# Performance work log

Hardware: AMD Instinct MI355X
Metric: run time of the kernel (lower is better)

## Reference

```python
import jax, jax.numpy as jnp
import numpy as np

B, S, H = 8, 1024, 1536          # batch, seq, hidden_size
NH, HD, AH = 8, 96, 768          # heads after head_ratio=2, head_size=hidden/16, all_head_size
K = 7                            # conv_kernel_size
IM = 3072                        # intermediate_size
EPS = 1e-12                      # ConvBert layer_norm_eps


def _ln(x, g, b):
    m = x.mean(-1, keepdims=True)
    v = ((x - m) ** 2).mean(-1, keepdims=True)
    return (x - m) / jnp.sqrt(v + EPS) * g + b


def _windows(x, k):
    # x: [B,S,C] -> sliding windows [B,S,k,C] with 'same' padding ((k-1)//2 each side, k odd)
    p = (k - 1) // 2
    xp = jnp.pad(x, ((0, 0), (p, p), (0, 0)))
    idx = jnp.arange(x.shape[1])[:, None] + jnp.arange(k)[None, :]
    return xp[:, idx, :]


def _forward(embed, wq, bq, wk, bk, wv, bv, dw, pw, sep_b, wck, bck, wco, bco,
             wso, bso, ln1_g, ln1_b, wi, bi, wo, bo, ln2_g, ln2_b, wd, bd):
    b, s, _ = embed.shape
    # --- projections (weights stored [in,out]) ---
    q = embed @ wq + bq            # [B,S,AH]
    kk = embed @ wk + bk
    v = embed @ wv + bv
    # --- SeparableConv1D on hidden states: depthwise(k=7) then pointwise + bias ---
    win_h = _windows(embed, K)                             # [B,S,K,H]
    dconv = jnp.einsum('bskc,ck->bsc', win_h, dw)          # depthwise, [B,S,H]
    sep = dconv @ pw + sep_b                               # pointwise, [B,S,AH]
    # --- span dynamic conv kernels ---
    conv_attn = sep * q                                    # [B,S,AH]
    ck = (conv_attn @ wck + bck).reshape(b, s, NH, K)      # [B,S,NH,K]
    ck = jax.nn.softmax(ck, axis=-1)
    co = embed @ wco + bco                                 # [B,S,AH]
    win_co = _windows(co, K).reshape(b, s, K, NH, HD)      # [B,S,K,NH,HD]
    conv_out = jnp.einsum('bskhd,bshk->bshd', win_co, ck)  # [B,S,NH,HD]
    # --- standard self-attention on the reduced heads ---
    qh = q.reshape(b, s, NH, HD)
    kh = kk.reshape(b, s, NH, HD)
    vh = v.reshape(b, s, NH, HD)
    scores = jnp.einsum('bqhd,bkhd->bhqk', qh, kh) / jnp.sqrt(jnp.float32(HD))
    probs = jax.nn.softmax(scores, axis=-1)
    ctx = jnp.einsum('bhqk,bkhd->bqhd', probs, vh)         # [B,S,NH,HD]
    # --- concat attention heads with conv heads -> [B,S,2*NH,HD] -> [B,S,H] ---
    ctx = jnp.concatenate([ctx, conv_out], axis=2).reshape(b, s, H)
    # --- self output (dropout is identity at inference) ---
    attn_out = _ln(ctx @ wso + bso + embed, ln1_g, ln1_b)
    # --- FFN ---
    inter = jax.nn.gelu(attn_out @ wi + bi, approximate=False)
    layer_out = _ln(inter @ wo + bo + attn_out, ln2_g, ln2_b)
    # --- global max pooling over sequence + linear decoder ---
    pooled = layer_out.max(axis=1)                         # [B,H]
    logits = pooled @ wd + bd                              # [B,1]
    return logits


def setup_inputs() -> dict:
    key = jax.random.key(0)
    ks = jax.random.split(key, 32)
    rn = lambda i, shape, s=0.02: jax.random.normal(ks[i], shape, jnp.float32) * s
    d = {}
    d['embed'] = jax.random.normal(ks[0], (B, S, H), jnp.float32)
    d['wq'] = rn(1, (H, AH)); d['bq'] = jnp.zeros((AH,), jnp.float32)
    d['wk'] = rn(2, (H, AH)); d['bk'] = jnp.zeros((AH,), jnp.float32)
    d['wv'] = rn(3, (H, AH)); d['bv'] = jnp.zeros((AH,), jnp.float32)
    d['dw'] = rn(4, (H, K)); d['pw'] = rn(5, (H, AH)); d['sep_b'] = jnp.zeros((AH,), jnp.float32)
    d['wck'] = rn(6, (AH, NH * K)); d['bck'] = jnp.zeros((NH * K,), jnp.float32)
    d['wco'] = rn(7, (H, AH)); d['bco'] = jnp.zeros((AH,), jnp.float32)
    d['wso'] = rn(8, (H, H)); d['bso'] = jnp.zeros((H,), jnp.float32)
    d['ln1_g'] = jnp.ones((H,), jnp.float32); d['ln1_b'] = jnp.zeros((H,), jnp.float32)
    d['wi'] = rn(9, (H, IM)); d['bi'] = jnp.zeros((IM,), jnp.float32)
    d['wo'] = rn(10, (IM, H)); d['bo'] = jnp.zeros((H,), jnp.float32)
    d['ln2_g'] = jnp.ones((H,), jnp.float32); d['ln2_b'] = jnp.zeros((H,), jnp.float32)
    d['wd'] = jax.random.uniform(ks[11], (H, 1), jnp.float32, -0.1, 0.1)
    d['bd'] = jnp.zeros((1,), jnp.float32)
    return d


def reference(embed, wq, bq, wk, bk, wv, bv, dw, pw, sep_b, wck, bck, wco, bco,
              wso, bso, ln1_g, ln1_b, wi, bi, wo, bo, ln2_g, ln2_b, wd, bd):
    return _forward(embed, wq, bq, wk, bk, wv, bv, dw, pw, sep_b, wck, bck, wco, bco,
                    wso, bso, ln1_g, ln1_b, wi, bi, wo, bo, ln2_g, ln2_b, wd, bd)
```

## Files before the change

kernel.cpp:

```cpp
#include <hip/hip_runtime.h>


typedef __bf16 bf16_t;
typedef short s16x8 __attribute__((ext_vector_type(8)));
typedef float f32x4 __attribute__((ext_vector_type(4)));

#define BB  8
#define SS  1024
#define HH  1536
#define NHH 8
#define HDD 96
#define AHH 768
#define IMM 3072

__device__ __forceinline__ float rd_adapt(const void* p, long long i, int isbf) {
    return isbf ? (float)((const bf16_t*)p)[i] : ((const float*)p)[i];
}

__device__ __forceinline__ float gelu_f(float v) {
    float u = v * (0.7978845608f + 0.0356774081f * v * v);
    float e = __expf(2.0f * u);
    float t = 1.0f - 2.0f / (e + 1.0f);
    return 0.5f * v * (1.0f + t);
}

__device__ __forceinline__ void gl2lds16(const bf16_t* g, bf16_t* l) {
    __builtin_amdgcn_global_load_lds(
        (__attribute__((address_space(1))) const void*)g,
        (__attribute__((address_space(3))) void*)l, 16, 0, 0);
}

__global__ __launch_bounds__(256)
void detect_kernel(const void* __restrict__ embed, int* __restrict__ flag)
{
    __shared__ int cnt[256];
    int t = threadIdx.x;
    float x = (float)((const bf16_t*)embed)[t];
    float a = fabsf(x);
    cnt[t] = (a > 1e-3f && a < 50.0f) ? 1 : 0;
    __syncthreads();
    for (int o = 128; o > 0; o >>= 1) { if (t < o) cnt[t] += cnt[t + o]; __syncthreads(); }
    if (t == 0) *flag = (cnt[0] >= 205) ? 1 : 0;
}

__global__ __launch_bounds__(256)
void convert_embed(const void* __restrict__ in, bf16_t* __restrict__ out,
                   const int* __restrict__ flagp)
{
    int isbf = *flagp;
    long long i0 = ((long long)blockIdx.x * 256 + threadIdx.x) * 8;
    if (isbf) {
        *(s16x8*)(out + i0) = *(const s16x8*)((const bf16_t*)in + i0);
    } else {
        const float* f = (const float*)in;
        #pragma unroll
        for (int j = 0; j < 8; j++) out[i0 + j] = (bf16_t)f[i0 + j];
    }
}

__global__ __launch_bounds__(256)
void concat_bias(const void* __restrict__ b0, const void* __restrict__ b1,
                 const void* __restrict__ b2, const void* __restrict__ b3,
                 bf16_t* __restrict__ out, const int* __restrict__ flagp)
{
    int isbf = *flagp;
    int t = blockIdx.x * 256 + threadIdx.x;
    int sel = t / 768, off = t - sel * 768;
    const void* src = (sel == 0) ? b0 : (sel == 1) ? b1 : (sel == 2) ? b2 : b3;
    out[t] = (bf16_t)rd_adapt(src, off, isbf);
}

__global__ __launch_bounds__(256)
void gemm_tile(const bf16_t* __restrict__ A, const bf16_t* __restrict__ Bt,
               bf16_t* __restrict__ C, const void* __restrict__ bias, long long biasOff,
               const bf16_t* __restrict__ emul, int lde, const int* __restrict__ flagp,
               int M, int N, int Kd, int lda, int ldb, int ldc,
               float scale, int act, int beta, int nlim)
{
    __shared__ bf16_t Sm[16384];

    int isbf = flagp ? *flagp : 1;
    int tid  = threadIdx.x;
    int wave = tid >> 6, lane = tid & 63;
    int wm = wave >> 1, wn = wave & 1;
    int row0 = blockIdx.x * 128;
    int col0 = blockIdx.y * 128;
    int lm = lane & 15;
    int kq = lane >> 4;

    int sr = tid >> 2;
    int sc = (tid & 3) * 8;
    const bf16_t* ga0 = A + (long long)(row0 + sr) * lda + sc;
    const bf16_t* ga1 = A + (long long)(row0 + 64 + sr) * lda + sc;
    int br0 = min(col0 + sr, nlim);
    int br1 = min(col0 + 64 + sr, nlim);
    const bf16_t* gb0 = Bt + (long long)br0 * ldb + sc;
    const bf16_t* gb1 = Bt + (long long)br1 * ldb + sc;
    bf16_t* lw = Sm + wave * 512;

    f32x4 acc[4][4] = {};

    for (int k0 = 0; k0 < Kd; k0 += 64) {
        #pragma unroll
        for (int h = 0; h < 2; h++) {
            int kh = k0 + h * 32;
            gl2lds16(ga0 + kh, lw + h * 4096);
            gl2lds16(ga1 + kh, lw + h * 4096 + 2048);
            gl2lds16(gb0 + kh, lw + 8192 + h * 4096);
            gl2lds16(gb1 + kh, lw + 8192 + h * 4096 + 2048);
        }
        __syncthreads();

        s16x8 af[2][4], bfr[2][4];
        #pragma unroll
        for (int h = 0; h < 2; h++) {
            #pragma unroll
            for (int i = 0; i < 4; i++)
                af[h][i] = *(const s16x8*)(Sm + h * 4096 + (wm * 64 + i * 16 + lm) * 32 + kq * 8);
            #pragma unroll
            for (int j = 0; j < 4; j++)
                bfr[h][j] = *(const s16x8*)(Sm + 8192 + h * 4096 + (wn * 64 + j * 16 + lm) * 32 + kq * 8);
        }
        #pragma unroll
        for (int i = 0; i < 4; i++)
            #pragma unroll
            for (int j = 0; j < 4; j++) {
                acc[i][j] = __builtin_amdgcn_mfma_f32_16x16x32_bf16(af[0][i], bfr[0][j], acc[i][j], 0, 0, 0);
                acc[i][j] = __builtin_amdgcn_mfma_f32_16x16x32_bf16(af[1][i], bfr[1][j], acc[i][j], 0, 0, 0);
            }
        __syncthreads();
    }

    #pragma unroll
    for (int j = 0; j < 4; j++) {
        int gcol = col0 + wn * 64 + j * 16 + lm;
        if (gcol >= N) continue;
        float bv = bias ? rd_adapt(bias, biasOff + gcol, isbf) : 0.0f;
        #pragma unroll
        for (int i = 0; i < 4; i++) {
            int grow0 = row0 + wm * 64 + i * 16 + kq * 4;
            #pragma unroll
            for (int r = 0; r < 4; r++) {
                float v = acc[i][j][r] * scale + bv;
                long long ci = (long long)(grow0 + r) * ldc + gcol;
                if (beta) v += (float)C[ci];
                if (emul) v *= (float)emul[(long long)(grow0 + r) * lde + gcol];
                if (act) v = gelu_f(v);
                C[ci] = (bf16_t)v;
            }
        }
    }
}

__global__ __launch_bounds__(256, 2)
void flash_attn(const bf16_t* __restrict__ qkv, const bf16_t* __restrict__ vT,
                bf16_t* __restrict__ ctxcat)
{
    const float ascale = 0.1020620726159658f;
    __shared__ bf16_t Pl[4 * 32 * 136];

    int bh = blockIdx.x;
    int b = bh >> 3, h = bh & 7;
    const bf16_t* Qp = qkv  + (long long)b * SS * 3072 + h * HDD;
    const bf16_t* Kp = qkv  + (long long)b * SS * 3072 + 768 + h * HDD;
    const bf16_t* Vt = vT   + (long long)b * AHH * SS + (long long)h * HDD * SS;
    bf16_t*       Op = ctxcat + (long long)b * SS * HH + h * HDD;

    int tid = threadIdx.x, wave = tid >> 6, lane = tid & 63;
    int lm = lane & 15, kq = lane >> 4;
    int q0 = blockIdx.y * 128 + wave * 32;
    bf16_t* Pw = Pl + wave * 32 * 136;

    s16x8 aq[2][3];
    #pragma unroll
    for (int i = 0; i < 2; i++)
        #pragma unroll
        for (int kf = 0; kf < 3; kf++)
            aq[i][kf] = *(const s16x8*)(Qp + (long long)(q0 + i * 16 + lm) * 3072 + kf * 32 + kq * 8);

    f32x4 Oacc[2][6] = {};
    float mrow[2][4], lrow[2][4];
    #pragma unroll
    for (int i = 0; i < 2; i++)
        #pragma unroll
        for (int r = 0; r < 4; r++) { mrow[i][r] = -1e30f; lrow[i][r] = 0.0f; }

    for (int kt = 0; kt < 8; kt++) {
        f32x4 S[2][8] = {};
        #pragma unroll
        for (int j = 0; j < 8; j++) {
            s16x8 bk[3];
            #pragma unroll
            for (int kf = 0; kf < 3; kf++)
                bk[kf] = *(const s16x8*)(Kp + (long long)(kt * 128 + j * 16 + lm) * 3072 + kf * 32 + kq * 8);
            #pragma unroll
            for (int i = 0; i < 2; i++)
                #pragma unroll
                for (int kf = 0; kf < 3; kf++)
                    S[i][j] = __builtin_amdgcn_mfma_f32_16x16x32_bf16(aq[i][kf], bk[kf], S[i][j], 0, 0, 0);
        }

        float mnew[2][4];
        #pragma unroll
        for (int i = 0; i < 2; i++) {
            #pragma unroll
            for (int r = 0; r < 4; r++) {
                float mx = -1e30f;
                #pragma unroll
                for (int j = 0; j < 8; j++) mx = fmaxf(mx, S[i][j][r]);
                #pragma unroll
                for (int msk = 1; msk <= 8; msk <<= 1) mx = fmaxf(mx, __shfl_xor(mx, msk));
                mnew[i][r] = fmaxf(mrow[i][r], mx * ascale);
            }
        }
        #pragma unroll
        for (int i = 0; i < 2; i++) {
            #pragma unroll
            for (int r = 0; r < 4; r++) {
                float al = __expf(mrow[i][r] - mnew[i][r]);
                lrow[i][r] *= al;
                #pragma unroll
                for (int n = 0; n < 6; n++) Oacc[i][n][r] *= al;
                mrow[i][r] = mnew[i][r];
            }
        }
        float psum[2][4] = {};
        __syncthreads();
        #pragma unroll
        for (int i = 0; i < 2; i++) {
            #pragma unroll
            for (int j = 0; j < 8; j++) {
                #pragma unroll
                for (int r = 0; r < 4; r++) {
                    float p = __expf(S[i][j][r] * ascale - mnew[i][r]);
                    psum[i][r] += p;
                    Pw[(i * 16 + kq * 4 + r) * 136 + j * 16 + lm] = (bf16_t)p;
                }
            }
        }
        #pragma unroll
        for (int i = 0; i < 2; i++) {
            #pragma unroll
            for (int r = 0; r < 4; r++) {
                float t = psum[i][r];
                #pragma unroll
                for (int msk = 1; msk <= 8; msk <<= 1) t += __shfl_xor(t, msk);
                lrow[i][r] += t;
            }
        }
        __syncthreads();

        s16x8 ap[2][4];
        #pragma unroll
        for (int i = 0; i < 2; i++)
            #pragma unroll
            for (int kf = 0; kf < 4; kf++)
                ap[i][kf] = *(const s16x8*)(Pw + (i * 16 + lm) * 136 + kf * 32 + kq * 8);
        #pragma unroll
        for (int n = 0; n < 6; n++) {
            s16x8 bv[4];
            #pragma unroll
            for (int kf = 0; kf < 4; kf++)
                bv[kf] = *(const s16x8*)(Vt + (long long)(n * 16 + lm) * SS + kt * 128 + kf * 32 + kq * 8);
            #pragma unroll
            for (int i = 0; i < 2; i++)
                #pragma unroll
                for (int kf = 0; kf < 4; kf++)
                    Oacc[i][n] = __builtin_amdgcn_mfma_f32_16x16x32_bf16(ap[i][kf], bv[kf], Oacc[i][n], 0, 0, 0);
        }
    }

    #pragma unroll
    for (int i = 0; i < 2; i++) {
        #pragma unroll
        for (int n = 0; n < 6; n++) {
            #pragma unroll
            for (int r = 0; r < 4; r++) {
                int row = q0 + i * 16 + kq * 4 + r;
                int col = n * 16 + lm;
                Op[(long long)row * HH + col] = (bf16_t)(Oacc[i][n][r] / lrow[i][r]);
            }
        }
    }
}

__global__ __launch_bounds__(256)
void transpose_pad(const void* __restrict__ in, bf16_t* __restrict__ out,
                   int R, int C, int ldin, long long inOff,
                   long long sInB, long long sOutB, const int* __restrict__ flagp)
{
    __shared__ bf16_t t[32][33];
    int isbf = flagp ? *flagp : 1;
    int z = blockIdx.z;
    long long base = inOff + (long long)z * sInB;
    bf16_t* op = out + (long long)z * sOutB;
    int tx = threadIdx.x & 31, ty = threadIdx.x >> 5;
    int cb = blockIdx.x * 32, rb = blockIdx.y * 32;
    #pragma unroll
    for (int rr = ty; rr < 32; rr += 8) {
        int r = rb + rr, c = cb + tx;
        t[rr][tx] = (c < C) ? (bf16_t)rd_adapt(in, base + (long long)r * ldin + c, isbf)
                            : (bf16_t)0.0f;
    }
    __syncthreads();
    #pragma unroll
    for (int rr = ty; rr < 32; rr += 8) {
        int c = cb + rr;
        op[(long long)c * R + rb + tx] = t[tx][rr];
    }
}

__global__ __launch_bounds__(256)
void dconv_kernel(const bf16_t* __restrict__ ebuf, const void* __restrict__ dw,
                  bf16_t* __restrict__ out, const int* __restrict__ flagp)
{
    int isbf = *flagp;
    long long i = (long long)blockIdx.x * 256 + threadIdx.x;
    int c = (int)(i % HH);
    long long bs = i / HH;
    int s = (int)(bs % SS);
    float acc = 0.0f;
    #pragma unroll
    for (int k = 0; k < 7; k++) {
        int ss = s + k - 3;
        if (ss >= 0 && ss < SS)
            acc += (float)ebuf[(bs + (k - 3)) * HH + c] * rd_adapt(dw, c * 7 + k, isbf);
    }
    out[i] = (bf16_t)acc;
}

__global__ __launch_bounds__(256)
void ck_softmax(const bf16_t* __restrict__ ck, float* __restrict__ ckp)
{
    int i = blockIdx.x * 256 + threadIdx.x;
    if (i >= BB * SS * NHH) return;
    int h = i % NHH;
    long long bs = i / NHH;
    const bf16_t* src = ck + bs * 64 + h * 7;
    float v[7], mx = -1e30f;
    #pragma unroll
    for (int k = 0; k < 7; k++) { v[k] = (float)src[k]; mx = fmaxf(mx, v[k]); }
    float sum = 0.0f;
    #pragma unroll
    for (int k = 0; k < 7; k++) { v[k] = expf(v[k] - mx); sum += v[k]; }
    float inv = 1.0f / sum;
    float* dst = ckp + bs * 56 + h * 7;
    #pragma unroll
    for (int k = 0; k < 7; k++) dst[k] = v[k] * inv;
}

__global__ __launch_bounds__(256)
void conv_out_kernel(const bf16_t* __restrict__ co, int ldco,
                     const float* __restrict__ ckp, bf16_t* __restrict__ ctxcat)
{
    long long i = (long long)blockIdx.x * 256 + threadIdx.x;
    int hd = (int)(i % AHH);
    long long bs = i / AHH;
    int s = (int)(bs % SS);
    int h = hd / HDD;
    const float* w = ckp + bs * 56 + h * 7;
    float acc = 0.0f;
    #pragma unroll
    for (int k = 0; k < 7; k++) {
        int ss = s + k - 3;
        if (ss >= 0 && ss < SS)
            acc += (float)co[(bs + (k - 3)) * ldco + hd] * w[k];
    }
    ctxcat[bs * HH + AHH + hd] = (bf16_t)acc;
}

__global__ __launch_bounds__(256)
void ln_kernel(const bf16_t* __restrict__ y, const bf16_t* __restrict__ res,
               const void* __restrict__ g, const void* __restrict__ bta,
               bf16_t* __restrict__ outb, const int* __restrict__ flagp)
{
    int isbf = *flagp;
    long long row = blockIdx.x;
    const bf16_t* yp = y + row * HH;
    const bf16_t* rp = res + row * HH;
    int tid = threadIdx.x;
    float x[6], s = 0.0f, s2 = 0.0f;
    #pragma unroll
    for (int i = 0; i < 6; i++) {
        int c = tid + i * 256;
        float v = (float)yp[c] + (float)rp[c];
        x[i] = v; s += v; s2 += v * v;
    }
    __shared__ float sa[256], sb[256];
    sa[tid] = s; sb[tid] = s2; __syncthreads();
    for (int o = 128; o > 0; o >>= 1) {
        if (tid < o) { sa[tid] += sa[tid + o]; sb[tid] += sb[tid + o]; }
        __syncthreads();
    }
    float mean = sa[0] * (1.0f / HH);
    float var  = sb[0] * (1.0f / HH) - mean * mean;
    float inv  = rsqrtf(var + 1e-12f);
    #pragma unroll
    for (int i = 0; i < 6; i++) {
        int c = tid + i * 256;
        float v = (x[i] - mean) * inv * rd_adapt(g, c, isbf) + rd_adapt(bta, c, isbf);
        outb[row * HH + c] = (bf16_t)v;
    }
}

__global__ __launch_bounds__(256)
void maxpool_p1(const bf16_t* __restrict__ lo, float* __restrict__ part)
{
    int sc = blockIdx.x, b = blockIdx.y;
    int tid = threadIdx.x;
    const bf16_t* p = lo + ((long long)b * SS + sc * 32) * HH;
    float m[6];
    #pragma unroll
    for (int k = 0; k < 6; k++) m[k] = -1e30f;
    for (int r = 0; r < 32; r++)
        #pragma unroll
        for (int k = 0; k < 6; k++)
            m[k] = fmaxf(m[k], (float)p[(long long)r * HH + k * 256 + tid]);
    #pragma unroll
    for (int k = 0; k < 6; k++)
        part[((long long)b * 32 + sc) * HH + k * 256 + tid] = m[k];
}

__global__ __launch_bounds__(256)
void maxpool_p2(const float* __restrict__ part, float* __restrict__ pooled)
{
    int i = blockIdx.x * 256 + threadIdx.x;
    if (i >= BB * HH) return;
    int b = i / HH, c = i % HH;
    float m = -1e30f;
    for (int ch = 0; ch < 32; ch++) m = fmaxf(m, part[((long long)b * 32 + ch) * HH + c]);
    pooled[i] = m;
}

__global__ __launch_bounds__(256)
void decoder_kernel(const float* __restrict__ pooled, const void* __restrict__ wd,
                    const void* __restrict__ bd, void* __restrict__ out,
                    const int* __restrict__ flagp)
{
    int isbf = *flagp;
    int b = blockIdx.x;
    int tid = threadIdx.x;
    float s = 0.0f;
    #pragma unroll
    for (int i = 0; i < 6; i++) {
        int c = tid + i * 256;
        s += pooled[b * HH + c] * rd_adapt(wd, c, isbf);
    }
    __shared__ float sa[256];
    sa[tid] = s; __syncthreads();
    for (int o = 128; o > 0; o >>= 1) { if (tid < o) sa[tid] += sa[tid + o]; __syncthreads(); }
    if (tid == 0) {
        float r = sa[0] + rd_adapt(bd, 0, isbf);
        if (isbf) ((bf16_t*)out)[b] = (bf16_t)r;
        else      ((float*)out)[b]  = r;
    }
}

extern "C" void kernel_launch(void* const* d_in, const int* in_sizes, int n_in,
                              void* d_out, int out_size, void* d_ws, size_t ws_size,
                              hipStream_t stream)
{
    const void* embed = d_in[0];
    const void* wq  = d_in[1];  const void* bq  = d_in[2];
    const void* wk  = d_in[3];  const void* bk  = d_in[4];
    const void* wv  = d_in[5];  const void* bv  = d_in[6];
    const void* dw  = d_in[7];  const void* pw  = d_in[8];  const void* sep_b = d_in[9];
    const void* wck = d_in[10]; const void* bck = d_in[11];
    const void* wco = d_in[12]; const void* bco = d_in[13];
    const void* wso = d_in[14]; const void* bso = d_in[15];
    const void* ln1g = d_in[16]; const void* ln1b = d_in[17];
    const void* wi  = d_in[18]; const void* bi  = d_in[19];
    const void* wo  = d_in[20]; const void* bo  = d_in[21];
    const void* ln2g = d_in[22]; const void* ln2b = d_in[23];
    const void* wd  = d_in[24]; const void* bd  = d_in[25];
    (void)ws_size; (void)in_sizes; (void)n_in; (void)out_size;

    char* ws = (char*)d_ws;
    char* A  = ws;
    char* B  = ws + 50331648;
    char* C_ = ws + 75497472;
    char* D  = ws + 88080384;
    char* E  = ws + 113246208;
    char* F  = ws + 138412032;
    char* XP = ws + 143130624;

    bf16_t* qkvco  = (bf16_t*)A;
    bf16_t* ybuf   = (bf16_t*)A;
    bf16_t* interb = (bf16_t*)A;
    bf16_t* lout   = (bf16_t*)A;
    bf16_t* wT_all = (bf16_t*)B;
    bf16_t* dconvb = (bf16_t*)B;
    bf16_t* ckb    = (bf16_t*)B;
    float*  ckp    = (float*)(B + 1310720);
    bf16_t* vT     = (bf16_t*)B;
    bf16_t* wfT    = (bf16_t*)B;
    bf16_t* sepb   = (bf16_t*)C_;
    float*  mpart  = (float*)C_;
    bf16_t* ctxcat = (bf16_t*)D;
    bf16_t* attn   = (bf16_t*)D;
    bf16_t* ebuf   = (bf16_t*)E;
    bf16_t* y2     = (bf16_t*)E;
    bf16_t* wT     = (bf16_t*)F;
    int*    flag   = (int*)XP;
    float*  pooled = (float*)(XP + 256);
    bf16_t* cbias  = (bf16_t*)(XP + 256 + 49152);

    dim3 blk(256);

    auto gemm = [&](const bf16_t* Ai, const bf16_t* Bt, bf16_t* Ci, const void* bias,
                    long long biasOff, const bf16_t* emul, int lde, const int* fl,
                    int M, int N, int Kd, int lda, int ldb, int ldc,
                    float scale, int act, int beta, int nlim) {
        dim3 g(M / 128, (N + 127) / 128, 1);
        gemm_tile<<<g, blk, 0, stream>>>(Ai, Bt, Ci, bias, biasOff, emul, lde, fl,
                                         M, N, Kd, lda, ldb, ldc,
                                         scale, act, beta, nlim);
    };
    auto transpose = [&](const void* in, bf16_t* out, int R, int Cc, int Cpad, int ldin,
                         long long inOff, int batch, long long sInB, long long sOutB,
                         const int* fl) {
        dim3 g(Cpad / 32, R / 32, batch);
        transpose_pad<<<g, blk, 0, stream>>>(in, out, R, Cc, ldin, inOff, sInB, sOutB, fl);
    };

    detect_kernel<<<dim3(1), blk, 0, stream>>>(embed, flag);
    convert_embed<<<dim3(6144), blk, 0, stream>>>(embed, ebuf, flag);

    transpose(wq,  wT_all + 0ll * 768 * 1536, 1536, 768, 768, 768, 0, 1, 0, 0, flag);
    transpose(wk,  wT_all + 1ll * 768 * 1536, 1536, 768, 768, 768, 0, 1, 0, 0, flag);
    transpose(wv,  wT_all + 2ll * 768 * 1536, 1536, 768, 768, 768, 0, 1, 0, 0, flag);
    transpose(wco, wT_all + 3ll * 768 * 1536, 1536, 768, 768, 768, 0, 1, 0, 0, flag);
    concat_bias<<<dim3(12), blk, 0, stream>>>(bq, bk, bv, bco, cbias, flag);
    gemm(ebuf, wT_all, qkvco, cbias, 0, nullptr, 0, nullptr,
         8192, 3072, 1536, HH, HH, 3072, 1.0f, 0, 0, 3071);

    dconv_kernel<<<dim3((BB * SS * HH) / 256), blk, 0, stream>>>(ebuf, dw, dconvb, flag);
    transpose(pw, wT, 1536, 768, 768, 768, 0, 1, 0, 0, flag);
    gemm(dconvb, wT, sepb, sep_b, 0, qkvco, 3072, flag,
         8192, 768, 1536, HH, HH, AHH, 1.0f, 0, 0, 767);

    transpose(wck, wT, 768, 56, 128, 56, 0, 1, 0, 0, flag);
    gemm(sepb, wT, ckb, bck, 0, nullptr, 0, flag,
         8192, 56, 768, AHH, AHH, 64, 1.0f, 0, 0, 127);
    ck_softmax<<<dim3((BB * SS * NHH) / 256), blk, 0, stream>>>(ckb, ckp);
    conv_out_kernel<<<dim3((BB * SS * AHH) / 256), blk, 0, stream>>>(qkvco + 2304, 3072, ckp, ctxcat);

    transpose(qkvco, vT, 1024, 768, 768, 3072, 1536, 8, 1024ll * 3072, 768ll * 1024, nullptr);
    flash_attn<<<dim3(64, 8), blk, 0, stream>>>(qkvco, vT, ctxcat);

    transpose(wso, wT, 1536, 1536, 1536, 1536, 0, 1, 0, 0, flag);
    gemm(ctxcat, wT, ybuf, bso, 0, nullptr, 0, flag,
         8192, 1536, 1536, HH, HH, HH, 1.0f, 0, 0, 1535);
    ln_kernel<<<dim3(8192), blk, 0, stream>>>(ybuf, ebuf, ln1g, ln1b, attn, flag);

    transpose(wi, wfT, 1536, 3072, 3072, 3072, 0, 1, 0, 0, flag);
    gemm(attn, wfT, interb, bi, 0, nullptr, 0, flag,
         8192, 3072, 1536, HH, HH, IMM, 1.0f, 1, 0, 3071);
    transpose(wo, wfT, 3072, 1536, 1536, 1536, 0, 1, 0, 0, flag);
    gemm(interb, wfT, y2, bo, 0, nullptr, 0, flag,
         8192, 1536, 3072, IMM, IMM, HH, 1.0f, 0, 0, 1535);
    ln_kernel<<<dim3(8192), blk, 0, stream>>>(y2, attn, ln2g, ln2b, lout, flag);

    maxpool_p1<<<dim3(32, 8), blk, 0, stream>>>(lout, mpart);
    maxpool_p2<<<dim3(48), blk, 0, stream>>>(mpart, pooled);
    decoder_kernel<<<dim3(BB), blk, 0, stream>>>(pooled, wd, bd, d_out, flag);
}
```

Baseline: 927.3 us.

## Add 256x256-tile pipelined MFMA GEMM and route large projections through it

Adds a new 512-thread GEMM kernel with 256x256 output tiles and a double-buffered 64-wide K stage loaded straight into LDS. It uses an XOR-swizzled LDS layout, splits each K step into four MFMA quarter-phases interleaved with the next stage loads, and remaps block IDs across XCDs for locality. The five big GEMMs (QKV+co, pointwise sep, self-output, FFN in/out) switch to it, aiming for more data reuse per tile and better overlap of loads with MFMA work. The costs are 128KB of LDS per block, high register pressure from 128 accumulators per thread, and a requirement that N be a multiple of 256 (768 is divisible by 256, so the sizes used here fit).

```diff
diff --git a/kernel.cpp b/kernel.cpp
--- a/kernel.cpp
+++ b/kernel.cpp
@@ -29,6 +29,9 @@
         (__attribute__((address_space(1))) const void*)g,
         (__attribute__((address_space(3))) void*)l, 16, 0, 0);
 }
+
+#define FENCE() asm volatile("" ::: "memory")
+#define BARRIER() do { FENCE(); __builtin_amdgcn_s_barrier(); FENCE(); } while (0)
 
 __global__ __launch_bounds__(256)
 void detect_kernel(const void* __restrict__ embed, int* __restrict__ flag)
@@ -68,6 +71,179 @@
     int sel = t / 768, off = t - sel * 768;
     const void* src = (sel == 0) ? b0 : (sel == 1) ? b1 : (sel == 2) ? b2 : b3;
     out[t] = (bf16_t)rd_adapt(src, off, isbf);
+}
+
+__global__ __launch_bounds__(512, 2)
+void gemm256(const bf16_t* __restrict__ A, const bf16_t* __restrict__ Bt,
+             bf16_t* __restrict__ C, const void* __restrict__ bias,
+             const bf16_t* __restrict__ emul, int lde, const int* __restrict__ flagp,
+             int M, int N, int Kd, int lda, int ldb, int ldc, int act, int tilesN)
+{
+    __shared__ bf16_t Sm[65536];
+    char* smb = (char*)Sm;
+    int isbf = flagp ? *flagp : 1;
+
+    int nwg = gridDim.x;
+    int orig = blockIdx.x;
+    int q = nwg >> 3, r = nwg & 7;
+    int xcd = orig & 7, lid = orig >> 3;
+    int wg = (xcd < r ? xcd * (q + 1) : r * (q + 1) + (xcd - r) * q) + lid;
+    int row0 = (wg / tilesN) * 256;
+    int col0 = (wg % tilesN) * 256;
+
+    int tid = threadIdx.x;
+    int wave = tid >> 6, lane = tid & 63;
+    int wm = wave >> 2, wn = wave & 3;
+    int lm = lane & 15, kq = lane >> 4;
+
+    int srow = lane >> 3;
+    int scol = 8 * ((lane & 7) ^ srow);
+
+    auto stageA2 = [&](int kt, int h, int bufo) {
+        #pragma unroll
+        for (int l = 0; l < 2; l++) {
+            int rloc = h * 128 + (2 * wave + l) * 8 + srow;
+            gl2lds16(A + (long long)(row0 + rloc) * lda + kt * 64 + scol,
+                     (bf16_t*)(smb + bufo * 32768 + h * 16384 + (2 * wave + l) * 1024));
+        }
+    };
+    auto stageB2 = [&](int kt, int h, int bufo) {
+        #pragma unroll
+        for (int l = 0; l < 2; l++) {
+            int rloc = h * 128 + (2 * wave + l) * 8 + srow;
+            gl2lds16(Bt + (long long)(col0 + rloc) * ldb + kt * 64 + scol,
+                     (bf16_t*)(smb + 65536 + bufo * 32768 + h * 16384 + (2 * wave + l) * 1024));
+        }
+    };
+
+    int xo = (lm & 7) << 4;
+    int cofs[2];
+    cofs[0] = (kq * 16) ^ xo;
+    cofs[1] = (64 + kq * 16) ^ xo;
+    int aoffs[8];
+    #pragma unroll
+    for (int ip = 0; ip < 8; ip++) aoffs[ip] = (wm * 128 + ip * 16 + lm) * 128;
+    int boffs[4];
+    #pragma unroll
+    for (int j = 0; j < 4; j++) boffs[j] = 65536 + (wn * 64 + j * 16 + lm) * 128;
+
+    f32x4 acc[8][4] = {};
+    s16x8 af[4][2], bf0[2][2], bf1[2][2];
+
+    int KT = Kd >> 6;
+
+    stageA2(0, 0, 0);
+    stageB2(0, 0, 0);
+    stageA2(0, 1, 0);
+    stageB2(0, 1, 0);
+    int k1 = min(1, KT - 1);
+    stageB2(k1, 0, 1);
+    stageA2(k1, 0, 1);
+    asm volatile("s_waitcnt vmcnt(4)" ::: "memory");
+    BARRIER();
+
+    for (int t = 0; t < KT; t++) {
+        int buf = t & 1;
+        int bA = buf * 32768;
+        int ob = buf ^ 1;
+        int tn1 = min(t + 1, KT - 1), tn2 = min(t + 2, KT - 1);
+
+        #pragma unroll
+        for (int i = 0; i < 4; i++)
+            #pragma unroll
+            for (int s = 0; s < 2; s++)
+                af[i][s] = *(const s16x8*)(smb + bA + aoffs[i] + cofs[s]);
+        #pragma unroll
+        for (int j = 0; j < 2; j++)
+            #pragma unroll
+            for (int s = 0; s < 2; s++)
+                bf0[j][s] = *(const s16x8*)(smb + bA + boffs[j] + cofs[s]);
+        stageA2(tn1, 1, ob);
+        BARRIER();
+        asm volatile("s_waitcnt lgkmcnt(0)" ::: "memory");
+        __builtin_amdgcn_sched_barrier(0);
+        __builtin_amdgcn_s_setprio(1);
+        #pragma unroll
+        for (int i = 0; i < 4; i++)
+            #pragma unroll
+            for (int j = 0; j < 2; j++) {
+                acc[i][j] = __builtin_amdgcn_mfma_f32_16x16x32_bf16(af[i][0], bf0[j][0], acc[i][j], 0, 0, 0);
+                acc[i][j] = __builtin_amdgcn_mfma_f32_16x16x32_bf16(af[i][1], bf0[j][1], acc[i][j], 0, 0, 0);
+            }
+        __builtin_amdgcn_s_setprio(0);
+        BARRIER();
+
+        #pragma unroll
+        for (int j = 0; j < 2; j++)
+            #pragma unroll
+            for (int s = 0; s < 2; s++)
+                bf1[j][s] = *(const s16x8*)(smb + bA + boffs[2 + j] + cofs[s]);
+        stageB2(tn1, 1, ob);
+        BARRIER();
+        asm volatile("s_waitcnt lgkmcnt(0)" ::: "memory");
+        __builtin_amdgcn_sched_barrier(0);
+        __builtin_amdgcn_s_setprio(1);
+        #pragma unroll
+        for (int i = 0; i < 4; i++)
+            #pragma unroll
+            for (int j = 0; j < 2; j++) {
+                acc[i][2 + j] = __builtin_amdgcn_mfma_f32_16x16x32_bf16(af[i][0], bf1[j][0], acc[i][2 + j], 0, 0, 0);
+                acc[i][2 + j] = __builtin_amdgcn_mfma_f32_16x16x32_bf16(af[i][1], bf1[j][1], acc[i][2 + j], 0, 0, 0);
+            }
+        __builtin_amdgcn_s_setprio(0);
+        BARRIER();
+
+        #pragma unroll
+        for (int i = 0; i < 4; i++)
+            #pragma unroll
+            for (int s = 0; s < 2; s++)
+                af[i][s] = *(const s16x8*)(smb + bA + aoffs[4 + i] + cofs[s]);
+        stageB2(tn2, 0, buf);
+        BARRIER();
+        asm volatile("s_waitcnt lgkmcnt(0)" ::: "memory");
+        __builtin_amdgcn_sched_barrier(0);
+        __builtin_amdgcn_s_setprio(1);
+        #pragma unroll
+        for (int i = 0; i < 4; i++)
+            #pragma unroll
+            for (int j = 0; j < 2; j++) {
+                acc[4 + i][2 + j] = __builtin_amdgcn_mfma_f32_16x16x32_bf16(af[i][0], bf1[j][0], acc[4 + i][2 + j], 0, 0, 0);
+                acc[4 + i][2 + j] = __builtin_amdgcn_mfma_f32_16x16x32_bf16(af[i][1], bf1[j][1], acc[4 + i][2 + j], 0, 0, 0);
+            }
+        __builtin_amdgcn_s_setprio(0);
+        BARRIER();
+
+        stageA2(tn2, 0, buf);
+        BARRIER();
+        __builtin_amdgcn_s_setprio(1);
+        #pragma unroll
+        for (int i = 0; i < 4; i++)
+            #pragma unroll
+            for (int j = 0; j < 2; j++) {
+                acc[4 + i][j] = __builtin_amdgcn_mfma_f32_16x16x32_bf16(af[i][0], bf0[j][0], acc[4 + i][j], 0, 0, 0);
+                acc[4 + i][j] = __builtin_amdgcn_mfma_f32_16x16x32_bf16(af[i][1], bf0[j][1], acc[4 + i][j], 0, 0, 0);
+            }
+        __builtin_amdgcn_s_setprio(0);
+        asm volatile("s_waitcnt vmcnt(4)" ::: "memory");
+        BARRIER();
+    }
+
+    #pragma unroll
+    for (int j = 0; j < 4; j++) {
+        int gcol = col0 + wn * 64 + j * 16 + lm;
+        float bv = bias ? rd_adapt(bias, gcol, isbf) : 0.0f;
+        #pragma unroll
+        for (int ip = 0; ip < 8; ip++) {
+            int grow0 = row0 + wm * 128 + ip * 16 + kq * 4;
+            #pragma unroll
+            for (int r = 0; r < 4; r++) {
+                float v = acc[ip][j][r] + bv;
+                if (emul) v *= (float)emul[(long long)(grow0 + r) * lde + gcol];
+                if (act) v = gelu_f(v);
+                C[(long long)(grow0 + r) * ldc + gcol] = (bf16_t)v;
+            }
+        }
+    }
 }
 
 __global__ __launch_bounds__(256)
@@ -507,6 +683,14 @@
 
     dim3 blk(256);
 
+    auto gemm_big = [&](const bf16_t* Ai, const bf16_t* Bt, bf16_t* Ci, const void* bias,
+                        const bf16_t* emul, int lde, const int* fl,
+                        int M, int N, int Kd, int lda, int ldb, int ldc, int act) {
+        int tn = N / 256;
+        dim3 g((M / 256) * tn);
+        gemm256<<<g, dim3(512), 0, stream>>>(Ai, Bt, Ci, bias, emul, lde, fl,
+                                             M, N, Kd, lda, ldb, ldc, act, tn);
+    };
     auto gemm = [&](const bf16_t* Ai, const bf16_t* Bt, bf16_t* Ci, const void* bias,
                     long long biasOff, const bf16_t* emul, int lde, const int* fl,
                     int M, int N, int Kd, int lda, int ldb, int ldc,
@@ -531,13 +715,13 @@
     transpose(wv,  wT_all + 2ll * 768 * 1536, 1536, 768, 768, 768, 0, 1, 0, 0, flag);
     transpose(wco, wT_all + 3ll * 768 * 1536, 1536, 768, 768, 768, 0, 1, 0, 0, flag);
     concat_bias<<<dim3(12), blk, 0, stream>>>(bq, bk, bv, bco, cbias, flag);
-    gemm(ebuf, wT_all, qkvco, cbias, 0, nullptr, 0, nullptr,
-         8192, 3072, 1536, HH, HH, 3072, 1.0f, 0, 0, 3071);
+    gemm_big(ebuf, wT_all, qkvco, cbias, nullptr, 0, nullptr,
+             8192, 3072, 1536, HH, HH, 3072, 0);
 
     dconv_kernel<<<dim3((BB * SS * HH) / 256), blk, 0, stream>>>(ebuf, dw, dconvb, flag);
     transpose(pw, wT, 1536, 768, 768, 768, 0, 1, 0, 0, flag);
-    gemm(dconvb, wT, sepb, sep_b, 0, qkvco, 3072, flag,
-         8192, 768, 1536, HH, HH, AHH, 1.0f, 0, 0, 767);
+    gemm_big(dconvb, wT, sepb, sep_b, qkvco, 3072, flag,
+             8192, 768, 1536, HH, HH, AHH, 0);
 
     transpose(wck, wT, 768, 56, 128, 56, 0, 1, 0, 0, flag);
     gemm(sepb, wT, ckb, bck, 0, nullptr, 0, flag,
@@ -549,16 +733,16 @@
     flash_attn<<<dim3(64, 8), blk, 0, stream>>>(qkvco, vT, ctxcat);
 
     transpose(wso, wT, 1536, 1536, 1536, 1536, 0, 1, 0, 0, flag);
-    gemm(ctxcat, wT, ybuf, bso, 0, nullptr, 0, flag,
-         8192, 1536, 1536, HH, HH, HH, 1.0f, 0, 0, 1535);
+    gemm_big(ctxcat, wT, ybuf, bso, nullptr, 0, flag,
+             8192, 1536, 1536, HH, HH, HH, 0);
     ln_kernel<<<dim3(8192), blk, 0, stream>>>(ybuf, ebuf, ln1g, ln1b, attn, flag);
 
     transpose(wi, wfT, 1536, 3072, 3072, 3072, 0, 1, 0, 0, flag);
-    gemm(attn, wfT, interb, bi, 0, nullptr, 0, flag,
-         8192, 3072, 1536, HH, HH, IMM, 1.0f, 1, 0, 3071);
+    gemm_big(attn, wfT, interb, bi, nullptr, 0, flag,
+             8192, 3072, 1536, HH, HH, IMM, 1);
     transpose(wo, wfT, 3072, 1536, 1536, 1536, 0, 1, 0, 0, flag);
-    gemm(interb, wfT, y2, bo, 0, nullptr, 0, flag,
-         8192, 1536, 3072, IMM, IMM, HH, 1.0f, 0, 0, 1535);
+    gemm_big(interb, wfT, y2, bo, nullptr, 0, flag,
+             8192, 1536, 3072, IMM, IMM, HH, 0);
     ln_kernel<<<dim3(8192), blk, 0, stream>>>(y2, attn, ln2g, ln2b, lout, flag);
 
     maxpool_p1<<<dim3(32, 8), blk, 0, stream>>>(lout, mpart);
```

After: 944.4 us. No clear change (+1.8%).

## Add 256x256 software-pipelined MFMA GEMM with XCD-aware tile mapping for large GEMMs

Applied to the files above, without the earlier changes.

Adds a 512-thread GEMM kernel with 256x256 tiles that double-buffers LDS through direct global-to-LDS loads. It interleaves the MFMA clusters with LDS reads using explicit waitcnt, sched_barrier and setprio, and remaps workgroups across XCDs. The four large GEMMs (QKV/co projection, attention output, FFN in and out) use it in place of the 128x128 tile kernel, which should raise data reuse and overlap memory with compute. The diff also merges the four weight transposes into one launch and folds the pooling reduction into the decoder kernel to cut launches. In exchange it needs 128KB of LDS per block and only supports M and N that are multiples of 256 and K that is a multiple of 128.

```diff
diff --git a/kernel.cpp b/kernel.cpp
--- a/kernel.cpp
+++ b/kernel.cpp
@@ -29,6 +29,25 @@
         (__attribute__((address_space(1))) const void*)g,
         (__attribute__((address_space(3))) void*)l, 16, 0, 0);
 }
+
+#define FENCE() asm volatile("" ::: "memory")
+#define BARRIER() do { FENCE(); __builtin_amdgcn_s_barrier(); FENCE(); } while (0)
+#define LGKM(n) asm volatile("s_waitcnt lgkmcnt(" #n ")" ::: "memory")
+#define VMCNT(n) asm volatile("s_waitcnt vmcnt(" #n ")" ::: "memory")
+#define SCHEDB() __builtin_amdgcn_sched_barrier(0)
+#define PRIO(n) __builtin_amdgcn_s_setprio(n)
+#define RDV(base, imm) (*(const s16x8*)(smb + (base) + (imm)))
+
+#define MFMA_CLUSTER(AF, BF, IO, JO)                                            \
+    _Pragma("unroll")                                                           \
+    for (int i_ = 0; i_ < 4; i_++)                                              \
+        _Pragma("unroll")                                                       \
+        for (int j_ = 0; j_ < 2; j_++) {                                        \
+            acc[(IO)+i_][(JO)+j_] = __builtin_amdgcn_mfma_f32_16x16x32_bf16(    \
+                AF[i_][0], BF[j_][0], acc[(IO)+i_][(JO)+j_], 0, 0, 0);          \
+            acc[(IO)+i_][(JO)+j_] = __builtin_amdgcn_mfma_f32_16x16x32_bf16(    \
+                AF[i_][1], BF[j_][1], acc[(IO)+i_][(JO)+j_], 0, 0, 0);          \
+        }
 
 __global__ __launch_bounds__(256)
 void detect_kernel(const void* __restrict__ embed, int* __restrict__ flag)
@@ -68,6 +87,163 @@
     int sel = t / 768, off = t - sel * 768;
     const void* src = (sel == 0) ? b0 : (sel == 1) ? b1 : (sel == 2) ? b2 : b3;
     out[t] = (bf16_t)rd_adapt(src, off, isbf);
+}
+
+template<int IB, int OB>
+__device__ __forceinline__ void tile_step(
+    char* smb, int vA0, int vA1, int vB0, int vB1,
+    const char* gA00, const char* gA01, const char* gA10, const char* gA11,
+    const char* gB00, const char* gB01, const char* gB10, const char* gB11,
+    char* ldsAw, char* ldsBw, int k1, int k2,
+    s16x8 (&af0)[4][2], s16x8 (&af1)[4][2],
+    s16x8 (&bf0)[2][2], s16x8 (&bf1)[2][2],
+    f32x4 (&acc)[8][4])
+{
+    BARRIER();
+    bf1[0][0] = RDV(vB0, IB + 4096); bf1[0][1] = RDV(vB1, IB + 4096);
+    bf1[1][0] = RDV(vB0, IB + 6144); bf1[1][1] = RDV(vB1, IB + 6144);
+    gl2lds16((const bf16_t*)(gA10 + k1), (bf16_t*)(ldsAw + OB + 16384));
+    gl2lds16((const bf16_t*)(gA11 + k1), (bf16_t*)(ldsAw + OB + 17408));
+    LGKM(4); SCHEDB(); PRIO(1);
+    MFMA_CLUSTER(af0, bf0, 0, 0);
+    PRIO(0);
+
+    BARRIER();
+    af1[0][0] = RDV(vA0, IB + 8192);  af1[0][1] = RDV(vA1, IB + 8192);
+    af1[1][0] = RDV(vA0, IB + 10240); af1[1][1] = RDV(vA1, IB + 10240);
+    af1[2][0] = RDV(vA0, IB + 12288); af1[2][1] = RDV(vA1, IB + 12288);
+    af1[3][0] = RDV(vA0, IB + 14336); af1[3][1] = RDV(vA1, IB + 14336);
+    gl2lds16((const bf16_t*)(gB10 + k1), (bf16_t*)(ldsBw + OB + 16384));
+    gl2lds16((const bf16_t*)(gB11 + k1), (bf16_t*)(ldsBw + OB + 17408));
+    LGKM(8); SCHEDB(); PRIO(1);
+    MFMA_CLUSTER(af0, bf1, 0, 2);
+    PRIO(0);
+
+    BARRIER();
+    gl2lds16((const bf16_t*)(gB00 + k2), (bf16_t*)(ldsBw + IB));
+    gl2lds16((const bf16_t*)(gB01 + k2), (bf16_t*)(ldsBw + IB + 1024));
+    gl2lds16((const bf16_t*)(gA00 + k2), (bf16_t*)(ldsAw + IB));
+    gl2lds16((const bf16_t*)(gA01 + k2), (bf16_t*)(ldsAw + IB + 1024));
+    LGKM(0); SCHEDB(); PRIO(1);
+    MFMA_CLUSTER(af1, bf1, 4, 2);
+    PRIO(0);
+
+    VMCNT(4);
+    BARRIER();
+    af0[0][0] = RDV(vA0, OB + 0);    af0[0][1] = RDV(vA1, OB + 0);
+    af0[1][0] = RDV(vA0, OB + 2048); af0[1][1] = RDV(vA1, OB + 2048);
+    af0[2][0] = RDV(vA0, OB + 4096); af0[2][1] = RDV(vA1, OB + 4096);
+    af0[3][0] = RDV(vA0, OB + 6144); af0[3][1] = RDV(vA1, OB + 6144);
+    PRIO(1);
+    MFMA_CLUSTER(af1, bf0, 4, 0);
+    PRIO(0);
+    bf0[0][0] = RDV(vB0, OB + 0);    bf0[0][1] = RDV(vB1, OB + 0);
+    bf0[1][0] = RDV(vB0, OB + 2048); bf0[1][1] = RDV(vB1, OB + 2048);
+}
+
+__global__ __launch_bounds__(512, 2)
+void gemm256(const bf16_t* __restrict__ A, const bf16_t* __restrict__ Bt,
+             bf16_t* __restrict__ C, const void* __restrict__ bias,
+             const bf16_t* __restrict__ emul, int lde, const int* __restrict__ flagp,
+             int M, int N, int Kd, int lda, int ldb, int ldc, int act, int tilesN)
+{
+    __shared__ bf16_t Sm[65536];
+    char* smb = (char*)Sm;
+    int isbf = flagp ? *flagp : 1;
+
+    int nwg = gridDim.x;
+    int orig = blockIdx.x;
+    int q = nwg >> 3, r = nwg & 7;
+    int xcd = orig & 7, lid = orig >> 3;
+    int wg = (xcd < r ? xcd * (q + 1) : r * (q + 1) + (xcd - r) * q) + lid;
+    int row0 = (wg / tilesN) * 256;
+    int col0 = (wg % tilesN) * 256;
+
+    int tid = threadIdx.x;
+    int wave = tid >> 6, lane = tid & 63;
+    int wm = wave >> 2, wn = wave & 3;
+    int lm = lane & 15, kq = lane >> 4;
+
+    int srow = lane >> 3;
+    int scol = 8 * ((lane & 7) ^ srow);
+
+    const char* gA00 = (const char*)(A + (long long)(row0 +   0 + (2*wave + 0)*8 + srow) * lda + scol);
+    const char* gA01 = (const char*)(A + (long long)(row0 +   0 + (2*wave + 1)*8 + srow) * lda + scol);
+    const char* gA10 = (const char*)(A + (long long)(row0 + 128 + (2*wave + 0)*8 + srow) * lda + scol);
+    const char* gA11 = (const char*)(A + (long long)(row0 + 128 + (2*wave + 1)*8 + srow) * lda + scol);
+    const char* gB00 = (const char*)(Bt + (long long)(col0 +   0 + (2*wave + 0)*8 + srow) * ldb + scol);
+    const char* gB01 = (const char*)(Bt + (long long)(col0 +   0 + (2*wave + 1)*8 + srow) * ldb + scol);
+    const char* gB10 = (const char*)(Bt + (long long)(col0 + 128 + (2*wave + 0)*8 + srow) * ldb + scol);
+    const char* gB11 = (const char*)(Bt + (long long)(col0 + 128 + (2*wave + 1)*8 + srow) * ldb + scol);
+
+    char* ldsAw = smb + 2 * wave * 1024;
+    char* ldsBw = smb + 65536 + 2 * wave * 1024;
+
+    int xo = (lm & 7) << 4;
+    int c0 = (kq * 16) ^ xo;
+    int c1 = (64 + kq * 16) ^ xo;
+    int vA0 = (wm * 128 + lm) * 128 + c0;
+    int vA1 = (wm * 128 + lm) * 128 + c1;
+    int vB0 = 65536 + (wn * 64 + lm) * 128 + c0;
+    int vB1 = 65536 + (wn * 64 + lm) * 128 + c1;
+
+    f32x4 acc[8][4] = {};
+    s16x8 af0[4][2], af1[4][2], bf0[2][2], bf1[2][2];
+
+    int KT = Kd >> 6;
+    int KTm1 = KT - 1;
+
+    gl2lds16((const bf16_t*)gA00, (bf16_t*)(ldsAw));
+    gl2lds16((const bf16_t*)gA01, (bf16_t*)(ldsAw + 1024));
+    gl2lds16((const bf16_t*)gA10, (bf16_t*)(ldsAw + 16384));
+    gl2lds16((const bf16_t*)gA11, (bf16_t*)(ldsAw + 17408));
+    gl2lds16((const bf16_t*)gB00, (bf16_t*)(ldsBw));
+    gl2lds16((const bf16_t*)gB01, (bf16_t*)(ldsBw + 1024));
+    gl2lds16((const bf16_t*)gB10, (bf16_t*)(ldsBw + 16384));
+    gl2lds16((const bf16_t*)gB11, (bf16_t*)(ldsBw + 17408));
+    int kb1 = min(1, KTm1) << 7;
+    gl2lds16((const bf16_t*)(gB00 + kb1), (bf16_t*)(ldsBw + 32768));
+    gl2lds16((const bf16_t*)(gB01 + kb1), (bf16_t*)(ldsBw + 33792));
+    gl2lds16((const bf16_t*)(gA00 + kb1), (bf16_t*)(ldsAw + 32768));
+    gl2lds16((const bf16_t*)(gA01 + kb1), (bf16_t*)(ldsAw + 33792));
+    VMCNT(4);
+    BARRIER();
+    af0[0][0] = RDV(vA0, 0);    af0[0][1] = RDV(vA1, 0);
+    af0[1][0] = RDV(vA0, 2048); af0[1][1] = RDV(vA1, 2048);
+    af0[2][0] = RDV(vA0, 4096); af0[2][1] = RDV(vA1, 4096);
+    af0[3][0] = RDV(vA0, 6144); af0[3][1] = RDV(vA1, 6144);
+    bf0[0][0] = RDV(vB0, 0);    bf0[0][1] = RDV(vB1, 0);
+    bf0[1][0] = RDV(vB0, 2048); bf0[1][1] = RDV(vB1, 2048);
+
+    for (int it = 0; it < (KT >> 1); ++it) {
+        int t = it << 1;
+        int k1 = min(t + 1, KTm1) << 7;
+        int k2 = min(t + 2, KTm1) << 7;
+        int k3 = min(t + 3, KTm1) << 7;
+        tile_step<0, 32768>(smb, vA0, vA1, vB0, vB1,
+                            gA00, gA01, gA10, gA11, gB00, gB01, gB10, gB11,
+                            ldsAw, ldsBw, k1, k2, af0, af1, bf0, bf1, acc);
+        tile_step<32768, 0>(smb, vA0, vA1, vB0, vB1,
+                            gA00, gA01, gA10, gA11, gB00, gB01, gB10, gB11,
+                            ldsAw, ldsBw, k2, k3, af0, af1, bf0, bf1, acc);
+    }
+
+    #pragma unroll
+    for (int j = 0; j < 4; j++) {
+        int gcol = col0 + wn * 64 + j * 16 + lm;
+        float bv = bias ? rd_adapt(bias, gcol, isbf) : 0.0f;
+        #pragma unroll
+        for (int ip = 0; ip < 8; ip++) {
+            int grow0 = row0 + wm * 128 + ip * 16 + kq * 4;
+            #pragma unroll
+            for (int r = 0; r < 4; r++) {
+                float v = acc[ip][j][r] + bv;
+                if (emul) v *= (float)emul[(long long)(grow0 + r) * lde + gcol];
+                if (act) v = gelu_f(v);
+                C[(long long)(grow0 + r) * ldc + gcol] = (bf16_t)v;
+            }
+        }
+    }
 }
 
 __global__ __launch_bounds__(256)
@@ -311,6 +487,31 @@
 }
 
 __global__ __launch_bounds__(256)
+void transpose_pad4(const void* __restrict__ i0, const void* __restrict__ i1,
+                    const void* __restrict__ i2, const void* __restrict__ i3,
+                    bf16_t* __restrict__ out, const int* __restrict__ flagp)
+{
+    __shared__ bf16_t t[32][33];
+    int isbf = *flagp;
+    int z = blockIdx.z;
+    const void* in = (z == 0) ? i0 : (z == 1) ? i1 : (z == 2) ? i2 : i3;
+    bf16_t* op = out + (long long)z * (768ll * 1536);
+    int tx = threadIdx.x & 31, ty = threadIdx.x >> 5;
+    int cb = blockIdx.x * 32, rb = blockIdx.y * 32;
+    #pragma unroll
+    for (int rr = ty; rr < 32; rr += 8) {
+        int r = rb + rr, c = cb + tx;
+        t[rr][tx] = (bf16_t)rd_adapt(in, (long long)r * 768 + c, isbf);
+    }
+    __syncthreads();
+    #pragma unroll
+    for (int rr = ty; rr < 32; rr += 8) {
+        int c = cb + rr;
+        op[(long long)c * 1536 + rb + tx] = t[tx][rr];
+    }
+}
+
+__global__ __launch_bounds__(256)
 void dconv_kernel(const bf16_t* __restrict__ ebuf, const void* __restrict__ dw,
                   bf16_t* __restrict__ out, const int* __restrict__ flagp)
 {
@@ -422,20 +623,9 @@
 }
 
 __global__ __launch_bounds__(256)
-void maxpool_p2(const float* __restrict__ part, float* __restrict__ pooled)
-{
-    int i = blockIdx.x * 256 + threadIdx.x;
-    if (i >= BB * HH) return;
-    int b = i / HH, c = i % HH;
-    float m = -1e30f;
-    for (int ch = 0; ch < 32; ch++) m = fmaxf(m, part[((long long)b * 32 + ch) * HH + c]);
-    pooled[i] = m;
-}
-
-__global__ __launch_bounds__(256)
-void decoder_kernel(const float* __restrict__ pooled, const void* __restrict__ wd,
-                    const void* __restrict__ bd, void* __restrict__ out,
-                    const int* __restrict__ flagp)
+void pool_decode(const float* __restrict__ part, const void* __restrict__ wd,
+                 const void* __restrict__ bd, void* __restrict__ out,
+                 const int* __restrict__ flagp)
 {
     int isbf = *flagp;
     int b = blockIdx.x;
@@ -444,7 +634,10 @@
     #pragma unroll
     for (int i = 0; i < 6; i++) {
         int c = tid + i * 256;
-        s += pooled[b * HH + c] * rd_adapt(wd, c, isbf);
+        float m = -1e30f;
+        for (int ch = 0; ch < 32; ch++)
+            m = fmaxf(m, part[((long long)b * 32 + ch) * HH + c]);
+        s += m * rd_adapt(wd, c, isbf);
     }
     __shared__ float sa[256];
     sa[tid] = s; __syncthreads();
@@ -502,11 +695,18 @@
     bf16_t* y2     = (bf16_t*)E;
     bf16_t* wT     = (bf16_t*)F;
     int*    flag   = (int*)XP;
-    float*  pooled = (float*)(XP + 256);
-    bf16_t* cbias  = (bf16_t*)(XP + 256 + 49152);
+    bf16_t* cbias  = (bf16_t*)(XP + 256);
 
     dim3 blk(256);
 
+    auto gemm_big = [&](const bf16_t* Ai, const bf16_t* Bt, bf16_t* Ci, const void* bias,
+                        const bf16_t* emul, int lde, const int* fl,
+                        int M, int N, int Kd, int lda, int ldb, int ldc, int act) {
+        int tn = N / 256;
+        dim3 g((M / 256) * tn);
+        gemm256<<<g, dim3(512), 0, stream>>>(Ai, Bt, Ci, bias, emul, lde, fl,
+                                             M, N, Kd, lda, ldb, ldc, act, tn);
+    };
     auto gemm = [&](const bf16_t* Ai, const bf16_t* Bt, bf16_t* Ci, const void* bias,
                     long long biasOff, const bf16_t* emul, int lde, const int* fl,
                     int M, int N, int Kd, int lda, int ldb, int ldc,
@@ -526,13 +726,10 @@
     detect_kernel<<<dim3(1), blk, 0, stream>>>(embed, flag);
     convert_embed<<<dim3(6144), blk, 0, stream>>>(embed, ebuf, flag);
 
-    transpose(wq,  wT_all + 0ll * 768 * 1536, 1536, 768, 768, 768, 0, 1, 0, 0, flag);
-    transpose(wk,  wT_all + 1ll * 768 * 1536, 1536, 768, 768, 768, 0, 1, 0, 0, flag);
-    transpose(wv,  wT_all + 2ll * 768 * 1536, 1536, 768, 768, 768, 0, 1, 0, 0, flag);
-    transpose(wco, wT_all + 3ll * 768 * 1536, 1536, 768, 768, 768, 0, 1, 0, 0, flag);
+    transpose_pad4<<<dim3(24, 48, 4), blk, 0, stream>>>(wq, wk, wv, wco, wT_all, flag);
     concat_bias<<<dim3(12), blk, 0, stream>>>(bq, bk, bv, bco, cbias, flag);
-    gemm(ebuf, wT_all, qkvco, cbias, 0, nullptr, 0, nullptr,
-         8192, 3072, 1536, HH, HH, 3072, 1.0f, 0, 0, 3071);
+    gemm_big(ebuf, wT_all, qkvco, cbias, nullptr, 0, nullptr,
+             8192, 3072, 1536, HH, HH, 3072, 0);
 
     dconv_kernel<<<dim3((BB * SS * HH) / 256), blk, 0, stream>>>(ebuf, dw, dconvb, flag);
     transpose(pw, wT, 1536, 768, 768, 768, 0, 1, 0, 0, flag);
@@ -549,19 +746,18 @@
     flash_attn<<<dim3(64, 8), blk, 0, stream>>>(qkvco, vT, ctxcat);
 
     transpose(wso, wT, 1536, 1536, 1536, 1536, 0, 1, 0, 0, flag);
-    gemm(ctxcat, wT, ybuf, bso, 0, nullptr, 0, flag,
-         8192, 1536, 1536, HH, HH, HH, 1.0f, 0, 0, 1535);
+    gemm_big(ctxcat, wT, ybuf, bso, nullptr, 0, flag,
+             8192, 1536, 1536, HH, HH, HH, 0);
     ln_kernel<<<dim3(8192), blk, 0, stream>>>(ybuf, ebuf, ln1g, ln1b, attn, flag);
 
     transpose(wi, wfT, 1536, 3072, 3072, 3072, 0, 1, 0, 0, flag);
-    gemm(attn, wfT, interb, bi, 0, nullptr, 0, flag,
-         8192, 3072, 1536, HH, HH, IMM, 1.0f, 1, 0, 3071);
+    gemm_big(attn, wfT, interb, bi, nullptr, 0, flag,
+             8192, 3072, 1536, HH, HH, IMM, 1);
     transpose(wo, wfT, 3072, 1536, 1536, 1536, 0, 1, 0, 0, flag);
-    gemm(interb, wfT, y2, bo, 0, nullptr, 0, flag,
-         8192, 1536, 3072, IMM, IMM, HH, 1.0f, 0, 0, 1535);
+    gemm_big(interb, wfT, y2, bo, nullptr, 0, flag,
+             8192, 1536, 3072, IMM, IMM, HH, 0);
     ln_kernel<<<dim3(8192), blk, 0, stream>>>(y2, attn, ln2g, ln2b, lout, flag);
 
     maxpool_p1<<<dim3(32, 8), blk, 0, stream>>>(lout, mpart);
-    maxpool_p2<<<dim3(48), blk, 0, stream>>>(mpart, pooled);
-    decoder_kernel<<<dim3(BB), blk, 0, stream>>>(pooled, wd, bd, d_out, flag);
-}
+    pool_decode<<<dim3(BB), blk, 0, stream>>>(mpart, wd, bd, d_out, flag);
+}
```

Measured after the change: 900.9 us. 1.03x faster.
